# Kernel optimization log

Measured on AMD Instinct MI355X. Metric: run time of the kernel, lower is better.

## Reference

```python
import jax, jax.numpy as jnp
import numpy as np

N = 4096            # tokens (dim 0 of x)
LATENT = 1024       # latent_vector_size
H = 16              # num_heads
DK = 64             # key_dim
DV = 64             # val_dim
MHK = H * DK        # 1024, width of q and k blocks


def setup_inputs() -> dict:
    key = jax.random.key(0)
    ks = jax.random.split(key, 5)
    return {
        "x": jax.random.normal(ks[0], (N, LATENT), dtype=jnp.float32),
        "w_qkv": jax.random.normal(ks[1], (LATENT, H * (2 * DK + DV)), dtype=jnp.float32) * (1.0 / np.sqrt(LATENT)),
        "b_qkv": jax.random.normal(ks[2], (H * (2 * DK + DV),), dtype=jnp.float32) * 0.01,
        "w_out": jax.random.normal(ks[3], (H * DV, LATENT), dtype=jnp.float32) * (1.0 / np.sqrt(H * DV)),
        "b_out": jax.random.normal(ks[4], (LATENT,), dtype=jnp.float32) * 0.01,
    }


def reference(x, w_qkv, b_qkv, w_out, b_out):
    # qkv projection: [N, H*(2*Dk+Dv)]
    qkv = x @ w_qkv + b_qkv
    # NOTE: the original module does NOT split into heads; q/k/v are the
    # concatenated head dims and a single [N, N] score matrix is formed,
    # scaled by sqrt(key_dim) (per-head dim), not sqrt(H*key_dim).
    q = qkv[:, :MHK]                 # [N, H*Dk]
    k = qkv[:, MHK:2 * MHK]          # [N, H*Dk]
    v = qkv[:, 2 * MHK:]             # [N, H*Dv]
    scores = (q @ k.T) * (1.0 / jnp.sqrt(jnp.float32(DK)))  # [N, N]
    attn = jax.nn.softmax(scores, axis=-1)
    out = attn @ v                   # [N, H*Dv]
    return out @ w_out + b_out       # [N, LATENT]
```

## Files before the change

kernel.cpp:

```cpp
#include <hip/hip_runtime.h>
#include <hip/hip_fp16.h>


typedef _Float16 half_t;
typedef _Float16 half8 __attribute__((ext_vector_type(8)));
typedef _Float16 half4 __attribute__((ext_vector_type(4)));
typedef float f32x4 __attribute__((ext_vector_type(4)));

static constexpr int N_TOK = 4096;
static constexpr int LATENT = 1024;
static constexpr int QKVN = 3072;

#define DEVI __device__ __forceinline__

DEVI void gld_lds16(const half_t* g, half_t* l) {
  __builtin_amdgcn_global_load_lds(
      (const __attribute__((address_space(1))) void*)g,
      (__attribute__((address_space(3))) void*)l,
      16, 0, 0);
}

DEVI f32x4 MFMA(half8 a, half8 b, f32x4 c) {
  return __builtin_amdgcn_mfma_f32_16x16x32_f16(a, b, c, 0, 0, 0);
}


DEVI void stageH(const half_t* __restrict__ g, int ld, half_t* lbase, int tid) {
#pragma unroll
  for (int i = 0; i < 2; ++i) {
    int c = tid + i * 512;
    int r = c >> 2;
    int k8 = ((c & 3) ^ ((r >> 1) & 3)) * 8;
    gld_lds16(g + (size_t)r * ld + k8, lbase + c * 8);
  }
}

template <int MODE>
__launch_bounds__(512, 2)
__global__ void gemm8(const half_t* __restrict__ A, int lda,
                      const half_t* __restrict__ B, int ldb,
                      void* __restrict__ Cout, int ldc,
                      const float* __restrict__ bias, int K) {
  __shared__ half_t Alds[2][2][256 * 32];
  __shared__ half_t Blds[2][2][256 * 32];

  const int tid = threadIdx.x;
  const int lane = tid & 63;
  const int wid = tid >> 6;

  const int nx = gridDim.x;
  const int nwg = nx * gridDim.y;
  const int bid = blockIdx.y * nx + blockIdx.x;
  const int cpx = nwg >> 3;
  const int swz = (bid & 7) * cpx + (bid >> 3);
  const int rowBlk = (swz / nx) * 256;
  const int colBlk = (swz % nx) * 256;

  const int wr = (wid >> 2) * 128;
  const int wc = (wid & 3) * 64;
  const int fr = lane & 15;
  const int fs = lane >> 4;

  const int kOff = blockIdx.z * K;
  const half_t* Ag = A + (size_t)rowBlk * lda + kOff;
  const half_t* Bg = B + (size_t)colBlk * ldb + kOff;

  f32x4 acc[8][4] = {};
  const int NT = K >> 6;

  stageH(Ag, lda, Alds[0][0], tid);
  stageH(Bg, ldb, Blds[0][0], tid);
  stageH(Ag + 32, lda, Alds[0][1], tid);
  stageH(Bg + 32, ldb, Blds[0][1], tid);
  asm volatile("s_waitcnt vmcnt(4)" ::: "memory");
  __builtin_amdgcn_s_barrier();

  for (int kt = 0; kt < NT; ++kt) {
    const int b = kt & 1;
    const bool st = (kt + 1 < NT);
    const half_t* AgN = Ag + (kt + 1) * 64;
    const half_t* BgN = Bg + (kt + 1) * 64;

    half8 af[8], bf[4];

#pragma unroll
    for (int kh = 0; kh < 2; ++kh) {
      const half_t* Ac = Alds[b][kh];
      const half_t* Bc = Blds[b][kh];
#pragma unroll
      for (int m = 0; m < 8; ++m) {
        int row = wr + m * 16 + fr;
        af[m] = *(const half8*)(Ac + row * 32 + ((fs ^ ((row >> 1) & 3)) * 8));
      }
#pragma unroll
      for (int n = 0; n < 4; ++n) {
        int row = wc + n * 16 + fr;
        bf[n] = *(const half8*)(Bc + row * 32 + ((fs ^ ((row >> 1) & 3)) * 8));
      }
      if (st) {
        stageH(AgN + kh * 32, lda, Alds[b ^ 1][kh], tid);
        stageH(BgN + kh * 32, ldb, Blds[b ^ 1][kh], tid);
      }
      __builtin_amdgcn_s_barrier();
      __builtin_amdgcn_s_setprio(1);
#pragma unroll
      for (int m = 0; m < 8; ++m)
#pragma unroll
        for (int n = 0; n < 4; ++n)
          acc[m][n] = MFMA(af[m], bf[n], acc[m][n]);
      __builtin_amdgcn_s_setprio(0);
      if (st) asm volatile("s_waitcnt vmcnt(4)" ::: "memory");
      else if (kh == 0) asm volatile("s_waitcnt vmcnt(0)" ::: "memory");
      __builtin_amdgcn_s_barrier();
    }
  }

  const size_t zoff = (MODE == 2) ? (size_t)blockIdx.z * N_TOK * ldc : 0;
#pragma unroll
  for (int m = 0; m < 8; ++m) {
#pragma unroll
    for (int n = 0; n < 4; ++n) {
#pragma unroll
      for (int j = 0; j < 4; ++j) {
        int row = rowBlk + wr + m * 16 + (lane >> 4) * 4 + j;
        int col = colBlk + wc + n * 16 + fr;
        float v = acc[m][n][j];
        if (MODE == 0) {
          v += bias[col];
          if (col < 1024) v *= 0.125f;
          ((half_t*)Cout)[(size_t)row * ldc + col] = (half_t)v;
        } else if (MODE == 1) {
          ((half_t*)Cout)[(size_t)row * ldc + col] = (half_t)v;
        } else {
          ((half_t*)Cout)[zoff + (size_t)row * ldc + col] = (half_t)v;
        }
      }
    }
  }
}

template <int ROWS>
DEVI void stage32(const half_t* __restrict__ g, int ld, half_t* lbase, int tid) {
#pragma unroll
  for (int c = tid; c < ROWS * 4; c += 256) {
    int r = c >> 2;
    int k8 = ((c & 3) ^ ((r >> 1) & 3)) * 8;
    gld_lds16(g + (size_t)r * ld + k8, lbase + c * 8);
  }
}

__launch_bounds__(256, 2)
__global__ void gemm2(const half_t* __restrict__ A, int lda,
                      const half_t* __restrict__ B, int ldb,
                      half_t* __restrict__ Cout, int ldc, int K) {
  constexpr int BM = 128, BN = 128, MF = 4, NF = 4;
  __shared__ half_t At[2][BM * 32];
  __shared__ half_t Bt[2][BN * 32];

  const int tid = threadIdx.x;
  const int lane = tid & 63;
  const int wid = tid >> 6;

  const int nx = gridDim.x;
  const int nwg = nx * gridDim.y;
  const int bid = blockIdx.y * nx + blockIdx.x;
  const int cpx = nwg >> 3;
  const int swz = (bid & 7) * cpx + (bid >> 3);
  const int rowBlk = (swz / nx) * BM;
  const int colBlk = (swz % nx) * BN;

  const int wr = (wid >> 1) * (BM / 2);
  const int wc = (wid & 1) * (BN / 2);
  const int fr = lane & 15;
  const int fs = lane >> 4;

  const half_t* Ag = A + (size_t)rowBlk * lda;
  const half_t* Bg = B + (size_t)colBlk * ldb;

  f32x4 acc[MF][NF] = {};
  const int NT = K >> 5;
  stage32<BM>(Ag, lda, At[0], tid);
  stage32<BN>(Bg, ldb, Bt[0], tid);
  __syncthreads();

  int cur = 0;
  for (int t = 0; t < NT; ++t) {
    if (t + 1 < NT) {
      stage32<BM>(Ag + (t + 1) * 32, lda, At[cur ^ 1], tid);
      stage32<BN>(Bg + (t + 1) * 32, ldb, Bt[cur ^ 1], tid);
    }
    const half_t* Ac = At[cur];
    const half_t* Bc = Bt[cur];
    half8 af[MF], bf[NF];
#pragma unroll
    for (int m = 0; m < MF; ++m) {
      int row = wr + m * 16 + fr;
      af[m] = *(const half8*)(Ac + row * 32 + ((fs ^ ((row >> 1) & 3)) * 8));
    }
#pragma unroll
    for (int n = 0; n < NF; ++n) {
      int row = wc + n * 16 + fr;
      bf[n] = *(const half8*)(Bc + row * 32 + ((fs ^ ((row >> 1) & 3)) * 8));
    }
#pragma unroll
    for (int m = 0; m < MF; ++m)
#pragma unroll
      for (int n = 0; n < NF; ++n)
        acc[m][n] = MFMA(af[m], bf[n], acc[m][n]);
    __syncthreads();
    cur ^= 1;
  }

#pragma unroll
  for (int m = 0; m < MF; ++m)
#pragma unroll
    for (int n = 0; n < NF; ++n)
#pragma unroll
      for (int j = 0; j < 4; ++j) {
        int row = rowBlk + wr + m * 16 + (lane >> 4) * 4 + j;
        int col = colBlk + wc + n * 16 + fr;
        Cout[(size_t)row * ldc + col] = (half_t)acc[m][n][j];
      }
}

__launch_bounds__(256)
__global__ void reduce_bias4(const half_t* __restrict__ p, const float* __restrict__ bias,
                             float* __restrict__ out) {
  int i = blockIdx.x * 256 + threadIdx.x;
  const size_t stride8 = (size_t)N_TOK * LATENT / 8;
  half8 a = ((const half8*)p)[i];
  half8 b = ((const half8*)p)[i + stride8];
  half8 c = ((const half8*)p)[i + 2 * stride8];
  half8 d = ((const half8*)p)[i + 3 * stride8];
  float4 e0 = ((const float4*)bias)[(i & 127) * 2];
  float4 e1 = ((const float4*)bias)[(i & 127) * 2 + 1];
  float r[8];
#pragma unroll
  for (int j = 0; j < 8; ++j)
    r[j] = (float)a[j] + (float)b[j] + (float)c[j] + (float)d[j];
  float4 o0, o1;
  o0.x = r[0] + e0.x; o0.y = r[1] + e0.y; o0.z = r[2] + e0.z; o0.w = r[3] + e0.w;
  o1.x = r[4] + e1.x; o1.y = r[5] + e1.y; o1.z = r[6] + e1.z; o1.w = r[7] + e1.w;
  ((float4*)out)[i * 2] = o0;
  ((float4*)out)[i * 2 + 1] = o1;
}

__launch_bounds__(256)
__global__ void softmax_rows(const half_t* __restrict__ S, half_t* __restrict__ P) {
  const int row = blockIdx.x;
  const int t = threadIdx.x;
  const half8* s8 = (const half8*)(S + (size_t)row * N_TOK);

  half8 v[2];
  float lmax = -1e30f;
#pragma unroll
  for (int i = 0; i < 2; ++i) {
    v[i] = s8[t + i * 256];
#pragma unroll
    for (int j = 0; j < 8; ++j) lmax = fmaxf(lmax, (float)v[i][j]);
  }
#pragma unroll
  for (int off = 32; off; off >>= 1) lmax = fmaxf(lmax, __shfl_xor(lmax, off));

  __shared__ float redm[4];
  __shared__ float reds[4];
  if ((t & 63) == 0) redm[t >> 6] = lmax;
  __syncthreads();
  lmax = fmaxf(fmaxf(redm[0], redm[1]), fmaxf(redm[2], redm[3]));

  float e[16];
  float lsum = 0.f;
#pragma unroll
  for (int i = 0; i < 2; ++i)
#pragma unroll
    for (int j = 0; j < 8; ++j) {
      float ev = __expf((float)v[i][j] - lmax);
      e[i * 8 + j] = ev;
      lsum += ev;
    }
#pragma unroll
  for (int off = 32; off; off >>= 1) lsum += __shfl_xor(lsum, off);
  if ((t & 63) == 0) reds[t >> 6] = lsum;
  __syncthreads();
  float inv = 1.f / (reds[0] + reds[1] + reds[2] + reds[3]);

  half8* p8 = (half8*)(P + (size_t)row * N_TOK);
#pragma unroll
  for (int i = 0; i < 2; ++i) {
    half8 h;
#pragma unroll
    for (int j = 0; j < 8; ++j) h[j] = (half_t)(e[i * 8 + j] * inv);
    p8[t + i * 256] = h;
  }
}

template <typename TI>
__global__ void transpose_to_f16(const TI* __restrict__ in, int ldin,
                                 half_t* __restrict__ out, int ldout) {
  __shared__ float tile[32][33];
  const int cb = blockIdx.x * 32;
  const int rb = blockIdx.y * 32;
  const int tx = threadIdx.x;
#pragma unroll
  for (int i = threadIdx.y; i < 32; i += 8)
    tile[i][tx] = (float)in[(size_t)(rb + i) * ldin + cb + tx];
  __syncthreads();
#pragma unroll
  for (int i = threadIdx.y; i < 32; i += 8)
    out[(size_t)(cb + i) * ldout + rb + tx] = (half_t)tile[tx][i];
}

__global__ void cvt_f32_f16(const float* __restrict__ in, half_t* __restrict__ out) {
  int i = blockIdx.x * 256 + threadIdx.x;
  float4 v = ((const float4*)in)[i];
  half4 h;
  h[0] = (half_t)v.x; h[1] = (half_t)v.y; h[2] = (half_t)v.z; h[3] = (half_t)v.w;
  ((half4*)out)[i] = h;
}

extern "C" void kernel_launch(void* const* d_in, const int* in_sizes, int n_in,
                              void* d_out, int out_size, void* d_ws, size_t ws_size,
                              hipStream_t stream) {
  const float* x = (const float*)d_in[0];
  const float* w_qkv = (const float*)d_in[1];
  const float* b_qkv = (const float*)d_in[2];
  const float* w_out = (const float*)d_in[3];
  const float* b_out = (const float*)d_in[4];
  float* out = (float*)d_out;

  char* ws = (char*)d_ws;
  half_t* xb    = (half_t*)(ws);
  half_t* wqkvT = (half_t*)(ws + ((size_t)8 << 20));
  half_t* qkv   = (half_t*)(ws + ((size_t)14 << 20));
  half_t* S     = (half_t*)(ws + ((size_t)46 << 20));
  half_t* P     = (half_t*)(ws + ((size_t)78 << 20));
  half_t* vwT   = (half_t*)(ws + ((size_t)118 << 20));
  half_t* woutT = (half_t*)(ws + ((size_t)126 << 20));
  half_t* parts = (half_t*)(ws + ((size_t)14 << 20));

  dim3 tb(32, 8);

  cvt_f32_f16<<<(N_TOK * LATENT) / (256 * 4), 256, 0, stream>>>(x, xb);
  transpose_to_f16<float><<<dim3(QKVN / 32, LATENT / 32), tb, 0, stream>>>(w_qkv, QKVN, wqkvT, LATENT);
  transpose_to_f16<float><<<dim3(LATENT / 32, LATENT / 32), tb, 0, stream>>>(w_out, LATENT, woutT, LATENT);
  gemm8<0><<<dim3(QKVN / 256, N_TOK / 256), 512, 0, stream>>>(
      xb, LATENT, wqkvT, LATENT, qkv, QKVN, b_qkv, LATENT);
  gemm2<<<dim3(N_TOK / 128, LATENT / 128), 256, 0, stream>>>(
      woutT, LATENT, qkv + 2 * LATENT, QKVN, vwT, N_TOK, LATENT);
  gemm8<1><<<dim3(N_TOK / 256, N_TOK / 256), 512, 0, stream>>>(
      qkv, QKVN, qkv + LATENT, QKVN, S, N_TOK, nullptr, LATENT);
  softmax_rows<<<N_TOK, 256, 0, stream>>>(S, P);
  gemm8<2><<<dim3(LATENT / 256, N_TOK / 256, 4), 512, 0, stream>>>(
      P, N_TOK, vwT, N_TOK, parts, LATENT, nullptr, 1024);
  reduce_bias4<<<(N_TOK * LATENT) / (256 * 8), 256, 0, stream>>>(parts, b_out, out);
}
```

Measured before the change: 172.6 us.

## Restructure GEMM main loop into 8-phase quadrant schedule with 64-wide K tiles

Changes the LDS layout from two 32-wide K halves to 128-row by 64-wide half tiles with an 8-way XOR swizzle. Splits each K step into four quadrant MFMA phases separated by barriers, with global-to-LDS staging of the next tiles interleaved between them. The intent is finer overlap of global loads, LDS reads and MFMA work with fewer live fragment registers. The trade-off is many more barriers and a loop that assumes an even tile count (NT/2 iterations) plus tricky vmcnt accounting.

```diff
diff --git a/kernel.cpp b/kernel.cpp
--- a/kernel.cpp
+++ b/kernel.cpp
@@ -25,15 +25,52 @@
 }
 
 
-DEVI void stageH(const half_t* __restrict__ g, int ld, half_t* lbase, int tid) {
+DEVI void stage_half(const half_t* __restrict__ g, int ld, half_t* dst, int tid) {
 #pragma unroll
   for (int i = 0; i < 2; ++i) {
     int c = tid + i * 512;
-    int r = c >> 2;
-    int k8 = ((c & 3) ^ ((r >> 1) & 3)) * 8;
-    gld_lds16(g + (size_t)r * ld + k8, lbase + c * 8);
-  }
-}
+    int r = c >> 3;
+    int s = c & 7;
+    gld_lds16(g + (size_t)r * ld + ((s ^ (r & 7)) * 8), dst + c * 8);
+  }
+}
+
+DEVI void rdA(half8 dst[4][2], const half_t* Ah, int mbase, int fr, int fs) {
+#pragma unroll
+  for (int mm = 0; mm < 4; ++mm) {
+    int rl = (mbase + mm) * 16 + fr;
+#pragma unroll
+    for (int kh = 0; kh < 2; ++kh)
+      dst[mm][kh] = *(const half8*)(Ah + rl * 64 + (((kh * 4 + fs) ^ (rl & 7)) * 8));
+  }
+}
+
+DEVI void rdB(half8 dst[2][2], const half_t* Bh, int rbase, int fr, int fs) {
+#pragma unroll
+  for (int nn = 0; nn < 2; ++nn) {
+    int rl = rbase + nn * 16 + fr;
+#pragma unroll
+    for (int kh = 0; kh < 2; ++kh)
+      dst[nn][kh] = *(const half8*)(Bh + rl * 64 + (((kh * 4 + fs) ^ (rl & 7)) * 8));
+  }
+}
+
+DEVI void mmq(f32x4 acc[8][4], half8 af[4][2], half8 bf[2][2], int mbase, int nbase) {
+#pragma unroll
+  for (int mm = 0; mm < 4; ++mm)
+#pragma unroll
+    for (int nn = 0; nn < 2; ++nn) {
+      f32x4 c = acc[mbase + mm][nbase + nn];
+      c = MFMA(af[mm][0], bf[nn][0], c);
+      c = MFMA(af[mm][1], bf[nn][1], c);
+      acc[mbase + mm][nbase + nn] = c;
+    }
+}
+
+#define BAR() __builtin_amdgcn_s_barrier()
+#define PRIO(x) __builtin_amdgcn_s_setprio(x)
+#define VMCNT6() asm volatile("s_waitcnt vmcnt(6)" ::: "memory")
+#define VMCNT0() asm volatile("s_waitcnt vmcnt(0)" ::: "memory")
 
 template <int MODE>
 __launch_bounds__(512, 2)
@@ -41,8 +78,8 @@
                       const half_t* __restrict__ B, int ldb,
                       void* __restrict__ Cout, int ldc,
                       const float* __restrict__ bias, int K) {
-  __shared__ half_t Alds[2][2][256 * 32];
-  __shared__ half_t Blds[2][2][256 * 32];
+  __shared__ half_t Al[2][2][128 * 64];
+  __shared__ half_t Bl[2][2][128 * 64];
 
   const int tid = threadIdx.x;
   const int lane = tid & 63;
@@ -60,59 +97,81 @@
   const int wc = (wid & 3) * 64;
   const int fr = lane & 15;
   const int fs = lane >> 4;
+  const int wcl = wc & 127;
+  const int bh = wc >> 7;
 
   const int kOff = blockIdx.z * K;
-  const half_t* Ag = A + (size_t)rowBlk * lda + kOff;
-  const half_t* Bg = B + (size_t)colBlk * ldb + kOff;
+  const half_t* AgH0 = A + (size_t)rowBlk * lda + kOff;
+  const half_t* AgH1 = A + (size_t)(rowBlk + 128) * lda + kOff;
+  const half_t* BgH0 = B + (size_t)colBlk * ldb + kOff;
+  const half_t* BgH1 = B + (size_t)(colBlk + 128) * ldb + kOff;
+
+  const half_t* myA0 = Al[0][wid >> 2];
+  const half_t* myA1 = Al[1][wid >> 2];
+  const half_t* myB0 = Bl[0][bh];
+  const half_t* myB1 = Bl[1][bh];
 
   f32x4 acc[8][4] = {};
+  half8 afA[4][2], afB[4][2], bf01[2][2], bf23[2][2];
+
   const int NT = K >> 6;
-
-  stageH(Ag, lda, Alds[0][0], tid);
-  stageH(Bg, ldb, Blds[0][0], tid);
-  stageH(Ag + 32, lda, Alds[0][1], tid);
-  stageH(Bg + 32, ldb, Blds[0][1], tid);
-  asm volatile("s_waitcnt vmcnt(4)" ::: "memory");
-  __builtin_amdgcn_s_barrier();
-
-  for (int kt = 0; kt < NT; ++kt) {
-    const int b = kt & 1;
-    const bool st = (kt + 1 < NT);
-    const half_t* AgN = Ag + (kt + 1) * 64;
-    const half_t* BgN = Bg + (kt + 1) * 64;
-
-    half8 af[8], bf[4];
-
-#pragma unroll
-    for (int kh = 0; kh < 2; ++kh) {
-      const half_t* Ac = Alds[b][kh];
-      const half_t* Bc = Blds[b][kh];
-#pragma unroll
-      for (int m = 0; m < 8; ++m) {
-        int row = wr + m * 16 + fr;
-        af[m] = *(const half8*)(Ac + row * 32 + ((fs ^ ((row >> 1) & 3)) * 8));
-      }
-#pragma unroll
-      for (int n = 0; n < 4; ++n) {
-        int row = wc + n * 16 + fr;
-        bf[n] = *(const half8*)(Bc + row * 32 + ((fs ^ ((row >> 1) & 3)) * 8));
-      }
-      if (st) {
-        stageH(AgN + kh * 32, lda, Alds[b ^ 1][kh], tid);
-        stageH(BgN + kh * 32, ldb, Blds[b ^ 1][kh], tid);
-      }
-      __builtin_amdgcn_s_barrier();
-      __builtin_amdgcn_s_setprio(1);
-#pragma unroll
-      for (int m = 0; m < 8; ++m)
-#pragma unroll
-        for (int n = 0; n < 4; ++n)
-          acc[m][n] = MFMA(af[m], bf[n], acc[m][n]);
-      __builtin_amdgcn_s_setprio(0);
-      if (st) asm volatile("s_waitcnt vmcnt(4)" ::: "memory");
-      else if (kh == 0) asm volatile("s_waitcnt vmcnt(0)" ::: "memory");
-      __builtin_amdgcn_s_barrier();
-    }
+  const int NI = NT >> 1;
+
+  stage_half(AgH0, lda, Al[0][0], tid);
+  stage_half(AgH1, lda, Al[0][1], tid);
+  stage_half(BgH0, ldb, Bl[0][0], tid);
+  stage_half(BgH1, ldb, Bl[0][1], tid);
+  stage_half(AgH0 + 64, lda, Al[1][0], tid);
+  stage_half(AgH1 + 64, lda, Al[1][1], tid);
+  stage_half(BgH0 + 64, ldb, Bl[1][0], tid);
+  VMCNT6();
+  BAR();
+
+  for (int i = 0; i < NI; ++i) {
+    const int t2 = 2 * i + 2;
+    const int t3 = 2 * i + 3;
+    const bool g2 = (t2 < NT);
+    const bool g3 = (t3 < NT);
+
+    rdA(afA, myA0, 0, fr, fs);
+    rdB(bf01, myB0, wcl, fr, fs);
+    stage_half(BgH1 + (size_t)(2 * i + 1) * 64, ldb, Bl[1][1], tid);
+    BAR(); PRIO(1); mmq(acc, afA, bf01, 0, 0); PRIO(0); BAR();
+
+    rdA(afB, myA0, 4, fr, fs);
+    BAR(); PRIO(1); mmq(acc, afB, bf01, 4, 0); PRIO(0); BAR();
+
+    rdB(bf23, myB0, wcl + 32, fr, fs);
+    if (g2) {
+      stage_half(AgH0 + (size_t)t2 * 64, lda, Al[0][0], tid);
+      stage_half(AgH1 + (size_t)t2 * 64, lda, Al[0][1], tid);
+    }
+    BAR(); PRIO(1); mmq(acc, afA, bf23, 0, 2); PRIO(0); BAR();
+
+    if (g2) stage_half(BgH0 + (size_t)t2 * 64, ldb, Bl[0][0], tid);
+    BAR(); PRIO(1); mmq(acc, afB, bf23, 4, 2); PRIO(0);
+    if (g2) VMCNT6(); else VMCNT0();
+    BAR();
+
+    rdA(afA, myA1, 0, fr, fs);
+    rdB(bf01, myB1, wcl, fr, fs);
+    if (g2) stage_half(BgH1 + (size_t)t2 * 64, ldb, Bl[0][1], tid);
+    BAR(); PRIO(1); mmq(acc, afA, bf01, 0, 0); PRIO(0); BAR();
+
+    rdA(afB, myA1, 4, fr, fs);
+    BAR(); PRIO(1); mmq(acc, afB, bf01, 4, 0); PRIO(0); BAR();
+
+    rdB(bf23, myB1, wcl + 32, fr, fs);
+    if (g3) {
+      stage_half(AgH0 + (size_t)t3 * 64, lda, Al[1][0], tid);
+      stage_half(AgH1 + (size_t)t3 * 64, lda, Al[1][1], tid);
+    }
+    BAR(); PRIO(1); mmq(acc, afA, bf23, 0, 2); PRIO(0); BAR();
+
+    if (g3) stage_half(BgH0 + (size_t)t3 * 64, ldb, Bl[1][0], tid);
+    BAR(); PRIO(1); mmq(acc, afB, bf23, 4, 2); PRIO(0);
+    if (g3) VMCNT6();
+    BAR();
   }
 
   const size_t zoff = (MODE == 2) ? (size_t)blockIdx.z * N_TOK * ldc : 0;
```

Result: slower. 178.1 us (+3.2%).

## Load B fragments directly from global into registers, dropping B LDS staging

Applied to the files above, without the earlier changes.

The GEMM kernel no longer stages the B tile through LDS. Each wave loads its B MFMA fragments straight from global memory into registers, double-buffered across the two k-halves, while A keeps its LDS double-buffered path. This removes half the LDS traffic and footprint, which may allow more occupancy or fewer bank conflicts. The cost is redundant global/L2 reads of B across the two row-waves and uncoalesced 16-byte per-lane loads, and the vmcnt accounting becomes more delicate.

```diff
diff --git a/kernel.cpp b/kernel.cpp
--- a/kernel.cpp
+++ b/kernel.cpp
@@ -24,6 +24,10 @@
   return __builtin_amdgcn_mfma_f32_16x16x32_f16(a, b, c, 0, 0, 0);
 }
 
+#define BAR() __builtin_amdgcn_s_barrier()
+#define PRIO(x) __builtin_amdgcn_s_setprio(x)
+#define VMCNT(n) asm volatile("s_waitcnt vmcnt(" #n ")" ::: "memory")
+
 
 DEVI void stageH(const half_t* __restrict__ g, int ld, half_t* lbase, int tid) {
 #pragma unroll
@@ -33,6 +37,12 @@
     int k8 = ((c & 3) ^ ((r >> 1) & 3)) * 8;
     gld_lds16(g + (size_t)r * ld + k8, lbase + c * 8);
   }
+}
+
+DEVI void loadB(half8 bf[4], const half_t* __restrict__ Blane, int ldb, int koff) {
+#pragma unroll
+  for (int n = 0; n < 4; ++n)
+    bf[n] = *(const half8*)(Blane + (size_t)n * 16 * ldb + koff);
 }
 
 template <int MODE>
@@ -42,7 +52,6 @@
                       void* __restrict__ Cout, int ldc,
                       const float* __restrict__ bias, int K) {
   __shared__ half_t Alds[2][2][256 * 32];
-  __shared__ half_t Blds[2][2][256 * 32];
 
   const int tid = threadIdx.x;
   const int lane = tid & 63;
@@ -60,59 +69,68 @@
   const int wc = (wid & 3) * 64;
   const int fr = lane & 15;
   const int fs = lane >> 4;
+  const int fs8 = fs * 8;
 
   const int kOff = blockIdx.z * K;
   const half_t* Ag = A + (size_t)rowBlk * lda + kOff;
-  const half_t* Bg = B + (size_t)colBlk * ldb + kOff;
+  const half_t* Blane = B + (size_t)(colBlk + wc + fr) * ldb + kOff;
 
   f32x4 acc[8][4] = {};
+  half8 af[8], bfK0[4], bfK1[4];
   const int NT = K >> 6;
 
+  loadB(bfK0, Blane, ldb, fs8);
   stageH(Ag, lda, Alds[0][0], tid);
-  stageH(Bg, ldb, Blds[0][0], tid);
   stageH(Ag + 32, lda, Alds[0][1], tid);
-  stageH(Bg + 32, ldb, Blds[0][1], tid);
-  asm volatile("s_waitcnt vmcnt(4)" ::: "memory");
-  __builtin_amdgcn_s_barrier();
+  VMCNT(0);
+  BAR();
 
   for (int kt = 0; kt < NT; ++kt) {
     const int b = kt & 1;
     const bool st = (kt + 1 < NT);
     const half_t* AgN = Ag + (kt + 1) * 64;
-    const half_t* BgN = Bg + (kt + 1) * 64;
-
-    half8 af[8], bf[4];
-
-#pragma unroll
-    for (int kh = 0; kh < 2; ++kh) {
-      const half_t* Ac = Alds[b][kh];
-      const half_t* Bc = Blds[b][kh];
+
+    loadB(bfK1, Blane, ldb, kt * 64 + 32 + fs8);
+    {
+      const half_t* Ac = Alds[b][0];
 #pragma unroll
       for (int m = 0; m < 8; ++m) {
         int row = wr + m * 16 + fr;
         af[m] = *(const half8*)(Ac + row * 32 + ((fs ^ ((row >> 1) & 3)) * 8));
       }
-#pragma unroll
-      for (int n = 0; n < 4; ++n) {
-        int row = wc + n * 16 + fr;
-        bf[n] = *(const half8*)(Bc + row * 32 + ((fs ^ ((row >> 1) & 3)) * 8));
+    }
+    if (st) stageH(AgN, lda, Alds[b ^ 1][0], tid);
+    BAR();
+    PRIO(1);
+#pragma unroll
+    for (int m = 0; m < 8; ++m)
+#pragma unroll
+      for (int n = 0; n < 4; ++n)
+        acc[m][n] = MFMA(af[m], bfK0[n], acc[m][n]);
+    PRIO(0);
+    if (st) VMCNT(6); else VMCNT(4);
+    BAR();
+
+    if (st) loadB(bfK0, Blane, ldb, (kt + 1) * 64 + fs8);
+    {
+      const half_t* Ac = Alds[b][1];
+#pragma unroll
+      for (int m = 0; m < 8; ++m) {
+        int row = wr + m * 16 + fr;
+        af[m] = *(const half8*)(Ac + row * 32 + ((fs ^ ((row >> 1) & 3)) * 8));
       }
-      if (st) {
-        stageH(AgN + kh * 32, lda, Alds[b ^ 1][kh], tid);
-        stageH(BgN + kh * 32, ldb, Blds[b ^ 1][kh], tid);
-      }
-      __builtin_amdgcn_s_barrier();
-      __builtin_amdgcn_s_setprio(1);
-#pragma unroll
-      for (int m = 0; m < 8; ++m)
-#pragma unroll
-        for (int n = 0; n < 4; ++n)
-          acc[m][n] = MFMA(af[m], bf[n], acc[m][n]);
-      __builtin_amdgcn_s_setprio(0);
-      if (st) asm volatile("s_waitcnt vmcnt(4)" ::: "memory");
-      else if (kh == 0) asm volatile("s_waitcnt vmcnt(0)" ::: "memory");
-      __builtin_amdgcn_s_barrier();
-    }
+    }
+    if (st) stageH(AgN + 32, lda, Alds[b ^ 1][1], tid);
+    BAR();
+    PRIO(1);
+#pragma unroll
+    for (int m = 0; m < 8; ++m)
+#pragma unroll
+      for (int n = 0; n < 4; ++n)
+        acc[m][n] = MFMA(af[m], bfK1[n], acc[m][n]);
+    PRIO(0);
+    if (st) VMCNT(6);
+    BAR();
   }
 
   const size_t zoff = (MODE == 2) ? (size_t)blockIdx.z * N_TOK * ldc : 0;
```

After: 231.4 us. +34.0%, slower.

## Switch GEMM LDS pipeline to a three-stage ring of 32-wide K tiles

Applied to the files above, without the earlier changes.

Replaces the double-buffered 64-wide K tile scheme (two 32-wide halves per buffer) with a triple-buffered ring of 32-wide K tiles prefetched two steps ahead. A and B loads are interleaved in one staging helper. This cuts shared memory per block and aims for a more uniform load/compute overlap with the same number of barriers per K step. It risks adding modulo-3 indexing overhead while giving little change in effective prefetch distance.

```diff
diff --git a/kernel.cpp b/kernel.cpp
--- a/kernel.cpp
+++ b/kernel.cpp
@@ -12,6 +12,9 @@
 static constexpr int QKVN = 3072;
 
 #define DEVI __device__ __forceinline__
+#define BAR() __builtin_amdgcn_s_barrier()
+#define PRIO(x) __builtin_amdgcn_s_setprio(x)
+#define VMCNT(n) asm volatile("s_waitcnt vmcnt(" #n ")" ::: "memory")
 
 DEVI void gld_lds16(const half_t* g, half_t* l) {
   __builtin_amdgcn_global_load_lds(
@@ -25,24 +28,27 @@
 }
 
 
-DEVI void stageH(const half_t* __restrict__ g, int ld, half_t* lbase, int tid) {
+DEVI void stageAB(const half_t* __restrict__ ga, int lda,
+                  const half_t* __restrict__ gb, int ldb,
+                  half_t* la, half_t* lb, int tid) {
 #pragma unroll
   for (int i = 0; i < 2; ++i) {
     int c = tid + i * 512;
     int r = c >> 2;
     int k8 = ((c & 3) ^ ((r >> 1) & 3)) * 8;
-    gld_lds16(g + (size_t)r * ld + k8, lbase + c * 8);
+    gld_lds16(ga + (size_t)r * lda + k8, la + c * 8);
+    gld_lds16(gb + (size_t)r * ldb + k8, lb + c * 8);
   }
 }
 
 template <int MODE>
 __launch_bounds__(512, 2)
-__global__ void gemm8(const half_t* __restrict__ A, int lda,
-                      const half_t* __restrict__ B, int ldb,
-                      void* __restrict__ Cout, int ldc,
-                      const float* __restrict__ bias, int K) {
-  __shared__ half_t Alds[2][2][256 * 32];
-  __shared__ half_t Blds[2][2][256 * 32];
+__global__ void gemm8h(const half_t* __restrict__ A, int lda,
+                       const half_t* __restrict__ B, int ldb,
+                       void* __restrict__ Cout, int ldc,
+                       const float* __restrict__ bias, int K) {
+  __shared__ half_t Alds[3][256 * 32];
+  __shared__ half_t Blds[3][256 * 32];
 
   const int tid = threadIdx.x;
   const int lane = tid & 63;
@@ -66,53 +72,45 @@
   const half_t* Bg = B + (size_t)colBlk * ldb + kOff;
 
   f32x4 acc[8][4] = {};
-  const int NT = K >> 6;
-
-  stageH(Ag, lda, Alds[0][0], tid);
-  stageH(Bg, ldb, Blds[0][0], tid);
-  stageH(Ag + 32, lda, Alds[0][1], tid);
-  stageH(Bg + 32, ldb, Blds[0][1], tid);
-  asm volatile("s_waitcnt vmcnt(4)" ::: "memory");
-  __builtin_amdgcn_s_barrier();
-
-  for (int kt = 0; kt < NT; ++kt) {
-    const int b = kt & 1;
-    const bool st = (kt + 1 < NT);
-    const half_t* AgN = Ag + (kt + 1) * 64;
-    const half_t* BgN = Bg + (kt + 1) * 64;
+  const int NT = K >> 5;
+
+  stageAB(Ag, lda, Bg, ldb, Alds[0], Blds[0], tid);
+  stageAB(Ag + 32, lda, Bg + 32, ldb, Alds[1], Blds[1], tid);
+  VMCNT(4);
+  BAR();
+
+  for (int t = 0; t < NT; ++t) {
+    const int b = t % 3;
+    const half_t* Ac = Alds[b];
+    const half_t* Bc = Blds[b];
 
     half8 af[8], bf[4];
-
-#pragma unroll
-    for (int kh = 0; kh < 2; ++kh) {
-      const half_t* Ac = Alds[b][kh];
-      const half_t* Bc = Blds[b][kh];
-#pragma unroll
-      for (int m = 0; m < 8; ++m) {
-        int row = wr + m * 16 + fr;
-        af[m] = *(const half8*)(Ac + row * 32 + ((fs ^ ((row >> 1) & 3)) * 8));
-      }
-#pragma unroll
-      for (int n = 0; n < 4; ++n) {
-        int row = wc + n * 16 + fr;
-        bf[n] = *(const half8*)(Bc + row * 32 + ((fs ^ ((row >> 1) & 3)) * 8));
-      }
-      if (st) {
-        stageH(AgN + kh * 32, lda, Alds[b ^ 1][kh], tid);
-        stageH(BgN + kh * 32, ldb, Blds[b ^ 1][kh], tid);
-      }
-      __builtin_amdgcn_s_barrier();
-      __builtin_amdgcn_s_setprio(1);
-#pragma unroll
-      for (int m = 0; m < 8; ++m)
-#pragma unroll
-        for (int n = 0; n < 4; ++n)
-          acc[m][n] = MFMA(af[m], bf[n], acc[m][n]);
-      __builtin_amdgcn_s_setprio(0);
-      if (st) asm volatile("s_waitcnt vmcnt(4)" ::: "memory");
-      else if (kh == 0) asm volatile("s_waitcnt vmcnt(0)" ::: "memory");
-      __builtin_amdgcn_s_barrier();
-    }
+#pragma unroll
+    for (int m = 0; m < 8; ++m) {
+      int row = wr + m * 16 + fr;
+      af[m] = *(const half8*)(Ac + row * 32 + ((fs ^ ((row >> 1) & 3)) * 8));
+    }
+#pragma unroll
+    for (int n = 0; n < 4; ++n) {
+      int row = wc + n * 16 + fr;
+      bf[n] = *(const half8*)(Bc + row * 32 + ((fs ^ ((row >> 1) & 3)) * 8));
+    }
+    if (t + 2 < NT) {
+      const int b2 = (t + 2) % 3;
+      stageAB(Ag + (t + 2) * 32, lda, Bg + (t + 2) * 32, ldb,
+              Alds[b2], Blds[b2], tid);
+    }
+    BAR();
+    PRIO(1);
+#pragma unroll
+    for (int m = 0; m < 8; ++m)
+#pragma unroll
+      for (int n = 0; n < 4; ++n)
+        acc[m][n] = MFMA(af[m], bf[n], acc[m][n]);
+    PRIO(0);
+    if (t + 2 < NT) VMCNT(4);
+    else if (t + 1 < NT) VMCNT(0);
+    BAR();
   }
 
   const size_t zoff = (MODE == 2) ? (size_t)blockIdx.z * N_TOK * ldc : 0;
@@ -343,14 +341,14 @@
   cvt_f32_f16<<<(N_TOK * LATENT) / (256 * 4), 256, 0, stream>>>(x, xb);
   transpose_to_f16<float><<<dim3(QKVN / 32, LATENT / 32), tb, 0, stream>>>(w_qkv, QKVN, wqkvT, LATENT);
   transpose_to_f16<float><<<dim3(LATENT / 32, LATENT / 32), tb, 0, stream>>>(w_out, LATENT, woutT, LATENT);
-  gemm8<0><<<dim3(QKVN / 256, N_TOK / 256), 512, 0, stream>>>(
+  gemm8h<0><<<dim3(QKVN / 256, N_TOK / 256), 512, 0, stream>>>(
       xb, LATENT, wqkvT, LATENT, qkv, QKVN, b_qkv, LATENT);
   gemm2<<<dim3(N_TOK / 128, LATENT / 128), 256, 0, stream>>>(
       woutT, LATENT, qkv + 2 * LATENT, QKVN, vwT, N_TOK, LATENT);
-  gemm8<1><<<dim3(N_TOK / 256, N_TOK / 256), 512, 0, stream>>>(
+  gemm8h<1><<<dim3(N_TOK / 256, N_TOK / 256), 512, 0, stream>>>(
       qkv, QKVN, qkv + LATENT, QKVN, S, N_TOK, nullptr, LATENT);
   softmax_rows<<<N_TOK, 256, 0, stream>>>(S, P);
-  gemm8<2><<<dim3(LATENT / 256, N_TOK / 256, 4), 512, 0, stream>>>(
+  gemm8h<2><<<dim3(LATENT / 256, N_TOK / 256, 4), 512, 0, stream>>>(
       P, N_TOK, vwT, N_TOK, parts, LATENT, nullptr, 1024);
   reduce_bias4<<<(N_TOK * LATENT) / (256 * 8), 256, 0, stream>>>(parts, b_out, out);
 }
```

Measured after the change: 175.1 us. Within noise of the previous version (+1.4%).
